# Kernel tuning notes

Hardware: AMD Instinct MI355X
Metric: run time of the kernel (lower is better)

## Reference

```python
import jax, jax.numpy as jnp
import numpy as np

TIME_SCALES = [1, 2, 4]
K = len(TIME_SCALES)      # 3 scales
N = 4                     # lcm(time_scales)
S = sum(TIME_SCALES)      # 7 slots
D_HEAD = 128              # d
D = S * D_HEAD            # 896
IO_DIM = 1024
RANK = 64
HIDDEN = 4 * D            # 3584
EPS = 1e-5


def _tables():
    active = np.empty((N, K), dtype=np.int64)
    perm = np.empty((N, K, N), dtype=np.int64)
    inv = np.empty((N, K, N), dtype=np.int64)
    ids = np.arange(N)
    for ph in range(N):
        off = 0
        for k, s in enumerate(TIME_SCALES):
            active[ph, k] = off + ph % s
            off += s
            j = ph % s
            alpha = N // s
            p = (ids + alpha * j) % N   # SHARED assignment
            perm[ph, k] = p
            ip = np.empty_like(p)
            ip[p] = ids
            inv[ph, k] = ip
    return active, perm, inv

ACTIVE, PERM, INV = _tables()


def _ln(x, scale, bias):
    mu = jnp.mean(x, axis=-1, keepdims=True)
    var = jnp.mean((x - mu) ** 2, axis=-1, keepdims=True)
    return (x - mu) * jax.lax.rsqrt(var + EPS) * scale + bias


def setup_inputs() -> dict:
    key = jax.random.key(0)
    ks = jax.random.split(key, 16)
    B, T = 8, 1024

    def w(k, shape, s=0.02):
        return jax.random.normal(k, shape, dtype=jnp.float32) * s

    return {
        "x": jax.random.normal(ks[0], (B, T, IO_DIM), dtype=jnp.float32),
        "enc_base_w": w(ks[1], (D, IO_DIM)),
        "enc_A_w": w(ks[2], (RANK, IO_DIM)),
        "enc_B": w(ks[3], (RANK, N, D)),
        "enc_beta": jnp.float32(0.01),
        "Wqkv": w(ks[4], (K, N, D_HEAD, 3 * D_HEAD)),
        "ln_attn_scale": jnp.ones((D_HEAD,), jnp.float32),
        "ln_attn_bias": jnp.zeros((D_HEAD,), jnp.float32),
        "ln_mixer_scale": jnp.ones((D,), jnp.float32),
        "ln_mixer_bias": jnp.zeros((D,), jnp.float32),
        "mixer_w1": w(ks[5], (HIDDEN, D)),
        "mixer_b1": jnp.zeros((HIDDEN,), jnp.float32),
        "mixer_w2": w(ks[6], (D, HIDDEN)),
        "mixer_b2": jnp.zeros((D,), jnp.float32),
        "dec_ln_scale": jnp.ones((N * D,), jnp.float32),
        "dec_ln_bias": jnp.zeros((N * D,), jnp.float32),
        "dec_down_w": w(ks[7], (RANK, N * D)),
        "dec_up_w": w(ks[8], (IO_DIM, RANK)),
        "phase": 1,
    }


def reference(x, enc_base_w, enc_A_w, enc_B, enc_beta, Wqkv,
              ln_attn_scale, ln_attn_bias, ln_mixer_scale, ln_mixer_bias,
              mixer_w1, mixer_b1, mixer_w2, mixer_b2,
              dec_ln_scale, dec_ln_bias, dec_down_w, dec_up_w, phase):
    B, T, _ = x.shape
    # ---- StreamLoRAEncoder: x [B,T,io] -> z0 [B,T,N,D]
    base = x @ enc_base_w.T                 # [B,T,D]
    h = x @ enc_A_w.T                       # [B,T,r]
    delta = jnp.einsum('btr,rnd->btnd', h, enc_B)
    z0 = base[:, :, None, :] + enc_beta * delta
    # ---- gather active slots for this phase (one slot per scale group)
    slots = ACTIVE[phase]                   # [K]
    z_slots = z0.reshape(B, T, N, S, D_HEAD)
    x_slot = z_slots[:, :, :, slots, :]     # [B,T,N,K,d]
    x_slot = _ln(x_slot, ln_attn_scale, ln_attn_bias)
    # ---- SHARED qkv projection (stream->head inverse perm, bmm, head->stream perm)
    x_in = x_slot.transpose(0, 1, 3, 2, 4)  # [B,T,K,N,d]
    kk = np.arange(K)[:, None]
    x_head = x_in[:, :, kk, INV[phase], :]  # [B,T,K,N,d]
    qkv = jnp.einsum('btknd,knde->btkne', x_head, Wqkv)  # [B,T,K,N,3d]
    qh, kh, vh = jnp.split(qkv, 3, axis=-1)
    p = PERM[phase]
    q = qh[:, :, kk, p, :].transpose(0, 3, 2, 1, 4).reshape(B, N * K, T, D_HEAD)
    k_ = kh[:, :, kk, p, :].transpose(0, 3, 2, 1, 4).reshape(B, N * K, T, D_HEAD)
    v = vh[:, :, kk, p, :].transpose(0, 3, 2, 1, 4).reshape(B, N * K, T, D_HEAD)
    # ---- causal attention over T per (stream, scale) head
    scores = jnp.einsum('bhtd,bhsd->bhts', q, k_) / np.float32(np.sqrt(D_HEAD))
    mask = jnp.tril(jnp.ones((T, T), dtype=bool))
    scores = jnp.where(mask, scores, jnp.float32(-1e9))
    attn = jax.nn.softmax(scores, axis=-1)
    out = jnp.einsum('bhts,bhsd->bhtd', attn, v)  # [B,N*K,T,d]
    # ---- scatter back to active slots (residual add)
    out5 = out.reshape(B, N, K, T, D_HEAD).transpose(0, 3, 1, 2, 4)  # [B,T,N,K,d]
    z1 = z_slots.at[:, :, :, slots, :].add(out5).reshape(B, T, N, D)
    # ---- mixer MLP (pre-LN residual)
    hm = _ln(z1, ln_mixer_scale, ln_mixer_bias)
    m = jax.nn.gelu(hm @ mixer_w1.T + mixer_b1, approximate=False) @ mixer_w2.T + mixer_b2
    z2 = z1 + m
    # ---- StreamLoRADecoder: concat streams, LN, rank-bottleneck projection
    cat = z2.reshape(B, T, N * D)
    y = _ln(cat, dec_ln_scale, dec_ln_bias) @ dec_down_w.T @ dec_up_w.T
    return y
```

## Files before the change

kernel.cpp:

```cpp
#include <hip/hip_runtime.h>
#include <hip/hip_bf16.h>
#include <math.h>


#define BT   8192
#define DH   128
#define DD   896
#define ND   3584
#define IO   1024
#define RK   64
#define HID  3584

typedef __attribute__((ext_vector_type(8))) short short8;
typedef __attribute__((ext_vector_type(4))) float f32x4;
typedef __hip_bfloat16 bf16;

#define DS_READ_B128(dst, p)                                                  \
    asm volatile("ds_read_b128 %0, %1"                                        \
                 : "=v"(dst)                                                  \
                 : "v"((const __attribute__((address_space(3))) bf16*)(p)))

__device__ __forceinline__ float gelu_f(float v)
{
    float u = v * 0.70710678118654752f;
    float a = fabsf(u);
    float t = __builtin_amdgcn_rcpf(1.0f + 0.3275911f * a);
    float p = t * (0.254829592f + t * (-0.284496736f + t * (1.421413741f +
              t * (-1.453152027f + t * 1.061405429f))));
    float er = 1.0f - p * __expf(-u * u);
    er = copysignf(er, u);
    return 0.5f * v * (1.0f + er);
}

template<int BM, int BN, int BK, int TM, int TN>
__global__ __launch_bounds__(256) void gemm_kernel(const float* __restrict__ A,
                                                   const float* __restrict__ B,
                                                   float* __restrict__ C,
                                                   int N, int Kd)
{
    constexpr int THREADS = (BM / TM) * (BN / TN);
    constexpr int LDA = BM + 4;
    constexpr int LDB = BN + 4;
    __shared__ float As[BK][LDA];
    __shared__ float Bs[BK][LDB];

    const int tid = threadIdx.x;
    constexpr int NX = BN / TN;
    const int tx = tid % NX;
    const int ty = tid / NX;
    const int row0 = blockIdx.y * BM;
    const int col0 = blockIdx.x * BN;

    float acc[TM][TN];
#pragma unroll
    for (int i = 0; i < TM; ++i)
#pragma unroll
        for (int j = 0; j < TN; ++j) acc[i][j] = 0.f;

    for (int k0 = 0; k0 < Kd; k0 += BK) {
        constexpr int AF4 = BM * BK / 4;
        for (int f = tid; f < AF4; f += THREADS) {
            int r  = f / (BK / 4);
            int c4 = (f % (BK / 4)) * 4;
            float4 v = *(const float4*)(A + (size_t)(row0 + r) * Kd + k0 + c4);
            As[c4 + 0][r] = v.x; As[c4 + 1][r] = v.y;
            As[c4 + 2][r] = v.z; As[c4 + 3][r] = v.w;
        }
        constexpr int BF4 = BN * BK / 4;
        for (int f = tid; f < BF4; f += THREADS) {
            int r  = f / (BK / 4);
            int c4 = (f % (BK / 4)) * 4;
            float4 v = *(const float4*)(B + (size_t)(col0 + r) * Kd + k0 + c4);
            Bs[c4 + 0][r] = v.x; Bs[c4 + 1][r] = v.y;
            Bs[c4 + 2][r] = v.z; Bs[c4 + 3][r] = v.w;
        }
        __syncthreads();

#pragma unroll
        for (int kk = 0; kk < BK; ++kk) {
            float a[TM], b[TN];
#pragma unroll
            for (int i = 0; i < TM; i += 4)
                *(float4*)&a[i] = *(const float4*)&As[kk][ty * TM + i];
#pragma unroll
            for (int j = 0; j < TN; j += 4)
                *(float4*)&b[j] = *(const float4*)&Bs[kk][tx * TN + j];
#pragma unroll
            for (int i = 0; i < TM; ++i)
#pragma unroll
                for (int j = 0; j < TN; ++j)
                    acc[i][j] = fmaf(a[i], b[j], acc[i][j]);
        }
        __syncthreads();
    }

    const int crow = row0 + ty * TM;
    const int ccol = col0 + tx * TN;
#pragma unroll
    for (int i = 0; i < TM; ++i) {
        float* cp = C + (size_t)(crow + i) * N + ccol;
#pragma unroll
        for (int j = 0; j < TN; ++j) cp[j] = acc[i][j];
    }
}

template<int SPLIT>
__global__ __launch_bounds__(256) void gemm_splitk_kernel(const float* __restrict__ A,
                                                          const float* __restrict__ B,
                                                          float* __restrict__ C,
                                                          int N, int ld)
{
    __shared__ float As[16][68];
    __shared__ float Bs[16][68];
    const int tid = threadIdx.x;
    const int tx = tid & 15, ty = tid >> 4;
    const int row0 = blockIdx.y * 64;
    const int col0 = blockIdx.x * 64;
    const int kn   = ld / SPLIT;
    const int kbeg = blockIdx.z * kn;

    float acc[4][4];
#pragma unroll
    for (int i = 0; i < 4; ++i)
#pragma unroll
        for (int j = 0; j < 4; ++j) acc[i][j] = 0.f;

    for (int k0 = kbeg; k0 < kbeg + kn; k0 += 16) {
        {
            int r = tid >> 2, c4 = (tid & 3) << 2;
            float4 v = *(const float4*)(A + (size_t)(row0 + r) * ld + k0 + c4);
            As[c4 + 0][r] = v.x; As[c4 + 1][r] = v.y;
            As[c4 + 2][r] = v.z; As[c4 + 3][r] = v.w;
            float4 w = *(const float4*)(B + (size_t)(col0 + r) * ld + k0 + c4);
            Bs[c4 + 0][r] = w.x; Bs[c4 + 1][r] = w.y;
            Bs[c4 + 2][r] = w.z; Bs[c4 + 3][r] = w.w;
        }
        __syncthreads();
#pragma unroll
        for (int kk = 0; kk < 16; ++kk) {
            float a[4], b[4];
            *(float4*)a = *(const float4*)&As[kk][ty * 4];
            *(float4*)b = *(const float4*)&Bs[kk][tx * 4];
#pragma unroll
            for (int i = 0; i < 4; ++i)
#pragma unroll
                for (int j = 0; j < 4; ++j)
                    acc[i][j] = fmaf(a[i], b[j], acc[i][j]);
        }
        __syncthreads();
    }

#pragma unroll
    for (int i = 0; i < 4; ++i)
#pragma unroll
        for (int j = 0; j < 4; ++j)
            atomicAdd(C + (size_t)(row0 + ty * 4 + i) * N + col0 + tx * 4 + j,
                      acc[i][j]);
}

template<int BN, int EPI>
__global__ __launch_bounds__(512, 2) void gemm_bf16_256(
    const bf16* __restrict__ A,
    const bf16* __restrict__ B,
    float* __restrict__ Cf,
    bf16* __restrict__ Cb,
    int N, int Kd,
    const float* __restrict__ bias)
{
    constexpr int NR    = BN / 64;
    constexpr int WTN   = 16 * NR;
    constexpr int ASLOT = 256 * 32;
    constexpr int BSLOT = BN * 32;
    __shared__ bf16 As[4 * ASLOT];
    __shared__ bf16 Bs[4 * BSLOT];

    const int tid  = threadIdx.x;
    const int wave = tid >> 6;
    const int lane = tid & 63;
    const int wm = wave >> 2, wn = wave & 3;
    const int lr = lane & 15, lq = lane >> 4;

    const int gx  = gridDim.x;
    int fid = blockIdx.y * gx + blockIdx.x;
    const int cpx = (gx * gridDim.y) >> 3;
    fid = (fid & 7) * cpx + (fid >> 3);
    const int row0 = (fid / gx) * 256;
    const int col0 = (fid % gx) * BN;

    const int sr  = lane >> 2;
    const int scs = (((lane & 3) ^ ((lane >> 3) & 3)) << 3);
    const bf16* Ag = A + (size_t)(row0 + sr) * Kd + scs;
    const bf16* Bg = B + (size_t)(col0 + sr) * Kd + scs;

    const int scox = (lq * 8) ^ (((lr >> 1) & 3) << 3);

    f32x4 acc[8][NR];
#pragma unroll
    for (int i = 0; i < 8; ++i)
#pragma unroll
        for (int j = 0; j < NR; ++j) acc[i][j] = (f32x4){0.f, 0.f, 0.f, 0.f};

    const int NH = Kd >> 5;

    auto stage = [&](int h) {
        const int slot = h & 3;
#pragma unroll
        for (int i = 0; i < 2; ++i) {
            const int rg = (i * 8 + wave) * 16;
            __builtin_amdgcn_global_load_lds(
                (const __attribute__((address_space(1))) unsigned int*)
                    (Ag + (size_t)rg * Kd + h * 32),
                (__attribute__((address_space(3))) unsigned int*)
                    (As + slot * ASLOT + rg * 32),
                16, 0, 0);
        }
#pragma unroll
        for (int i = 0; i < BN / 128; ++i) {
            const int rg = (i * 8 + wave) * 16;
            __builtin_amdgcn_global_load_lds(
                (const __attribute__((address_space(1))) unsigned int*)
                    (Bg + (size_t)rg * Kd + h * 32),
                (__attribute__((address_space(3))) unsigned int*)
                    (Bs + slot * BSLOT + rg * 32),
                16, 0, 0);
        }
    };

    stage(0); stage(1); stage(2);

    for (int h = 0; h < NH; ++h) {
        if (h + 3 < NH) stage(h + 3);

        const int ahead = NH - 1 - h;
        if constexpr (BN == 256) {
            if (ahead >= 3)      asm volatile("s_waitcnt vmcnt(12)" ::: "memory");
            else if (ahead == 2) asm volatile("s_waitcnt vmcnt(8)"  ::: "memory");
            else if (ahead == 1) asm volatile("s_waitcnt vmcnt(4)"  ::: "memory");
            else                 asm volatile("s_waitcnt vmcnt(0)"  ::: "memory");
        } else {
            if (ahead >= 3)      asm volatile("s_waitcnt vmcnt(9)"  ::: "memory");
            else if (ahead == 2) asm volatile("s_waitcnt vmcnt(6)"  ::: "memory");
            else if (ahead == 1) asm volatile("s_waitcnt vmcnt(3)"  ::: "memory");
            else                 asm volatile("s_waitcnt vmcnt(0)"  ::: "memory");
        }
        __builtin_amdgcn_s_barrier();

        const bf16* Ab = As + (h & 3) * ASLOT;
        const bf16* Bb = Bs + (h & 3) * BSLOT;

        short8 bfr[NR], afr[8];
#pragma unroll
        for (int nt = 0; nt < NR; ++nt)
            DS_READ_B128(bfr[nt], Bb + (wn * WTN + nt * 16 + lr) * 32 + scox);
#pragma unroll
        for (int mt = 0; mt < 8; ++mt)
            DS_READ_B128(afr[mt], Ab + (wm * 128 + mt * 16 + lr) * 32 + scox);

        asm volatile("s_waitcnt lgkmcnt(0)" ::: "memory");
        __builtin_amdgcn_sched_barrier(0);

        __builtin_amdgcn_s_setprio(1);
#pragma unroll
        for (int mt = 0; mt < 8; ++mt)
#pragma unroll
            for (int nt = 0; nt < NR; ++nt)
                acc[mt][nt] = __builtin_amdgcn_mfma_f32_16x16x32_bf16(
                    afr[mt], bfr[nt], acc[mt][nt], 0, 0, 0);
        __builtin_amdgcn_s_setprio(0);

        __builtin_amdgcn_s_barrier();
    }

#pragma unroll
    for (int mt = 0; mt < 8; ++mt) {
#pragma unroll
        for (int nt = 0; nt < NR; ++nt) {
            const int col = col0 + wn * WTN + nt * 16 + lr;
            const float bcol = (EPI == 0) ? 0.f : bias[col];
#pragma unroll
            for (int r = 0; r < 4; ++r) {
                const int row = row0 + wm * 128 + mt * 16 + lq * 4 + r;
                float v = acc[mt][nt][r] + bcol;
                if (EPI == 1) {
                    Cb[(size_t)row * N + col] = __float2bfloat16(gelu_f(v));
                } else if (EPI == 2) {
                    Cf[(size_t)row * N + col] += v;
                } else {
                    Cf[(size_t)row * N + col] = v;
                }
            }
        }
    }
}

__global__ __launch_bounds__(256) void pack_enc_kernel(const float* __restrict__ baseW,
                                                       const float* __restrict__ Aw,
                                                       const float* __restrict__ Bv,
                                                       const float* __restrict__ betap,
                                                       bf16* __restrict__ outp)
{
    __shared__ float Ps[64][68];
    __shared__ float Qs[64][68];
    const int tid = threadIdx.x;
    const int e0 = blockIdx.y * 64;
    const int k0 = blockIdx.x * 64;

    for (int f = tid; f < 1024; f += 256) {
        int r = f >> 4, c4 = (f & 15) << 2;
        *(float4*)&Ps[r][c4] = *(const float4*)(Bv + (size_t)r * ND + e0 + c4);
        *(float4*)&Qs[r][c4] = *(const float4*)(Aw + (size_t)r * IO + k0 + c4);
    }
    __syncthreads();

    const int tx = tid & 15, ty = tid >> 4;
    float acc[4][4];
#pragma unroll
    for (int i = 0; i < 4; ++i)
#pragma unroll
        for (int j = 0; j < 4; ++j) acc[i][j] = 0.f;

#pragma unroll 8
    for (int r = 0; r < 64; ++r) {
        float a[4], b[4];
        *(float4*)a = *(const float4*)&Ps[r][ty * 4];
        *(float4*)b = *(const float4*)&Qs[r][tx * 4];
#pragma unroll
        for (int i = 0; i < 4; ++i)
#pragma unroll
            for (int j = 0; j < 4; ++j) acc[i][j] = fmaf(a[i], b[j], acc[i][j]);
    }

    const float beta = betap[0];
#pragma unroll
    for (int i = 0; i < 4; ++i) {
        const int e = e0 + ty * 4 + i;
        const int d = e % DD;
#pragma unroll
        for (int j = 0; j < 4; ++j) {
            const int k = k0 + tx * 4 + j;
            float v = baseW[(size_t)d * IO + k] + beta * acc[i][j];
            outp[(size_t)e * IO + k] = __float2bfloat16(v);
        }
    }
}

__global__ __launch_bounds__(256) void qkv_bf16_kernel(
    const bf16* __restrict__ xh,
    const bf16* __restrict__ Wt,
    bf16* __restrict__ Qg,
    bf16* __restrict__ Kg,
    bf16* __restrict__ Vtg,
    const int* __restrict__ phase_p,
    int go)
{
    __shared__ bf16 As[128 * 64];
    __shared__ bf16 Bs[128 * 64];

    const int ph  = phase_p[0] & 3;
    const int zbl = blockIdx.z;
    const int hh  = (go + zbl) % 12;
    const int n   = hh / 3;
    const int k   = hh % 3;
    const int m   = (k == 0) ? n
                  : (k == 1) ? ((n + 2 * (ph & 1)) & 3)
                             : ((n + (ph & 3)) & 3);
    const bf16* A  = xh + (size_t)zbl * (1024 * 128);
    const bf16* Bw = Wt + (size_t)(k * 4 + m) * (384 * 128);

    const int tid  = threadIdx.x;
    const int wave = tid >> 6;
    const int lane = tid & 63;
    const int wm = wave >> 1, wn = wave & 1;
    const int row0 = blockIdx.y * 128;
    const int col0 = blockIdx.x * 128;
    const int lr = lane & 15;
    const int lq = lane >> 4;
    const int srow = lane >> 3;
    const int scol = (lane & 7) * 8;

    f32x4 acc[4][4];
#pragma unroll
    for (int i = 0; i < 4; ++i)
#pragma unroll
        for (int j = 0; j < 4; ++j) acc[i][j] = (f32x4){0.f, 0.f, 0.f, 0.f};

#pragma unroll
    for (int k0 = 0; k0 < 128; k0 += 64) {
#pragma unroll
        for (int j = 0; j < 4; ++j) {
            const int rg = wave * 32 + j * 8;
            __builtin_amdgcn_global_load_lds(
                (const __attribute__((address_space(1))) unsigned int*)
                    (A + (size_t)(row0 + rg + srow) * 128 + k0 + scol),
                (__attribute__((address_space(3))) unsigned int*)(As + rg * 64),
                16, 0, 0);
        }
#pragma unroll
        for (int j = 0; j < 4; ++j) {
            const int rg = wave * 32 + j * 8;
            __builtin_amdgcn_global_load_lds(
                (const __attribute__((address_space(1))) unsigned int*)
                    (Bw + (size_t)(col0 + rg + srow) * 128 + k0 + scol),
                (__attribute__((address_space(3))) unsigned int*)(Bs + rg * 64),
                16, 0, 0);
        }
        __syncthreads();

#pragma unroll
        for (int s = 0; s < 64; s += 32) {
            short8 af[4], bf[4];
#pragma unroll
            for (int mt = 0; mt < 4; ++mt)
                af[mt] = *(const short8*)&As[(wm * 64 + mt * 16 + lr) * 64 + s + lq * 8];
#pragma unroll
            for (int nt = 0; nt < 4; ++nt)
                bf[nt] = *(const short8*)&Bs[(wn * 64 + nt * 16 + lr) * 64 + s + lq * 8];
#pragma unroll
            for (int mt = 0; mt < 4; ++mt)
#pragma unroll
                for (int nt = 0; nt < 4; ++nt)
                    acc[mt][nt] = __builtin_amdgcn_mfma_f32_16x16x32_bf16(
                        af[mt], bf[nt], acc[mt][nt], 0, 0, 0);
        }
        __syncthreads();
    }

    if (col0 < 256) {
        bf16* C = (col0 == 0 ? Qg : Kg) + (size_t)zbl * (1024 * 128);
#pragma unroll
        for (int mt = 0; mt < 4; ++mt)
#pragma unroll
            for (int nt = 0; nt < 4; ++nt) {
                const int col = wn * 64 + nt * 16 + lr;
#pragma unroll
                for (int r = 0; r < 4; ++r) {
                    const int row = row0 + wm * 64 + mt * 16 + lq * 4 + r;
                    C[(size_t)row * 128 + col] = __float2bfloat16(acc[mt][nt][r]);
                }
            }
    } else {
        bf16* Vt = Vtg + (size_t)zbl * (128 * 1024);
#pragma unroll
        for (int mt = 0; mt < 4; ++mt)
#pragma unroll
            for (int nt = 0; nt < 4; ++nt) {
                const int d = wn * 64 + nt * 16 + lr;
                const int rowb = row0 + wm * 64 + mt * 16 + lq * 4;
                union { bf16 h[4]; uint2 u; } pk;
#pragma unroll
                for (int r = 0; r < 4; ++r)
                    pk.h[r] = __float2bfloat16(acc[mt][nt][r]);
                *(uint2*)(Vt + (size_t)d * 1024 + rowb) = pk.u;
            }
    }
}

__global__ __launch_bounds__(256) void flash_bf16_kernel(
    const bf16* __restrict__ Qg,
    const bf16* __restrict__ Kg,
    const bf16* __restrict__ Vtg,
    float* __restrict__ z,
    const int* __restrict__ phase_p,
    int go)
{
    __shared__ bf16 Ks[64 * 128];
    __shared__ bf16 Vs[128 * 64];
    __shared__ bf16 Ps[64 * 64];

    const int ph  = phase_p[0] & 3;
    const int zbl = blockIdx.x;
    const int zb  = go + zbl;
    const int b   = zb / 12;
    const int hh  = zb % 12;
    const int n   = hh / 3;
    const int ks  = hh % 3;
    const int slot = (ks == 0) ? 0 : (ks == 1 ? 1 + (ph & 1) : 3 + (ph & 3));
    const int q0  = blockIdx.y * 64;

    const bf16* Qp = Qg  + (size_t)zbl * (1024 * 128);
    const bf16* Kp = Kg  + (size_t)zbl * (1024 * 128);
    const bf16* Vp = Vtg + (size_t)zbl * (128 * 1024);

    const int tid  = threadIdx.x;
    const int wave = tid >> 6;
    const int lane = tid & 63;
    const int lr = lane & 15;
    const int lq = lane >> 4;
    const int sr4 = lane >> 4, sc4 = (lane & 15) * 8;
    const int sr8 = lane >> 3, sc8 = (lane & 7) * 8;
    const int swz = (lr & 7) << 3;

    short8 qreg[4];
#pragma unroll
    for (int s = 0; s < 4; ++s)
        qreg[s] = *(const short8*)(Qp + (size_t)(q0 + wave * 16 + lr) * 128
                                   + s * 32 + lq * 8);

    f32x4 accO[8];
    float m_i[4], l_i[4];
#pragma unroll
    for (int j = 0; j < 8; ++j) accO[j] = (f32x4){0.f, 0.f, 0.f, 0.f};
#pragma unroll
    for (int r = 0; r < 4; ++r) { m_i[r] = -1e30f; l_i[r] = 0.f; }
    const float sc = 0.08838834764831845f;

    for (int j0 = 0; j0 <= q0; j0 += 64) {
#pragma unroll
        for (int j = 0; j < 4; ++j) {
            const int rg = wave * 16 + j * 4;
            const int krow = rg + sr4;
            const int kcol = sc4 ^ ((krow & 7) << 3);
            __builtin_amdgcn_global_load_lds(
                (const __attribute__((address_space(1))) unsigned int*)
                    (Kp + (size_t)(j0 + krow) * 128 + kcol),
                (__attribute__((address_space(3))) unsigned int*)(Ks + rg * 128),
                16, 0, 0);
        }
#pragma unroll
        for (int j = 0; j < 4; ++j) {
            const int rg = wave * 32 + j * 8;
            const int vrow = rg + sr8;
            const int vcol = sc8 ^ ((vrow & 7) << 3);
            __builtin_amdgcn_global_load_lds(
                (const __attribute__((address_space(1))) unsigned int*)
                    (Vp + (size_t)vrow * 1024 + j0 + vcol),
                (__attribute__((address_space(3))) unsigned int*)(Vs + rg * 64),
                16, 0, 0);
        }
        __syncthreads();

        f32x4 accS[4];
#pragma unroll
        for (int nt = 0; nt < 4; ++nt) accS[nt] = (f32x4){0.f, 0.f, 0.f, 0.f};
#pragma unroll
        for (int s = 0; s < 4; ++s) {
            short8 bk[4];
#pragma unroll
            for (int nt = 0; nt < 4; ++nt)
                bk[nt] = *(const short8*)&Ks[(nt * 16 + lr) * 128
                                             + ((s * 32 + lq * 8) ^ swz)];
#pragma unroll
            for (int nt = 0; nt < 4; ++nt)
                accS[nt] = __builtin_amdgcn_mfma_f32_16x16x32_bf16(
                    qreg[s], bk[nt], accS[nt], 0, 0, 0);
        }

        const bool need_mask = (j0 == q0);
#pragma unroll
        for (int r = 0; r < 4; ++r) {
            const int row = q0 + wave * 16 + lq * 4 + r;
            float sv[4];
#pragma unroll
            for (int nt = 0; nt < 4; ++nt) {
                float v = accS[nt][r] * sc;
                if (need_mask && (j0 + nt * 16 + lr > row)) v = -1e30f;
                sv[nt] = v;
            }
            float mx = fmaxf(fmaxf(sv[0], sv[1]), fmaxf(sv[2], sv[3]));
#pragma unroll
            for (int msk = 8; msk; msk >>= 1) mx = fmaxf(mx, __shfl_xor(mx, msk, 16));
            float mnew = fmaxf(m_i[r], mx);
            float al   = __expf(m_i[r] - mnew);
            float rs = 0.f;
#pragma unroll
            for (int nt = 0; nt < 4; ++nt) {
                sv[nt] = __expf(sv[nt] - mnew);
                rs += sv[nt];
            }
#pragma unroll
            for (int msk = 8; msk; msk >>= 1) rs += __shfl_xor(rs, msk, 16);
            l_i[r] = l_i[r] * al + rs;
            m_i[r] = mnew;
#pragma unroll
            for (int d8 = 0; d8 < 8; ++d8) accO[d8][r] *= al;
            const int prow = wave * 16 + lq * 4 + r;
            const int pswz = (prow & 7) << 3;
#pragma unroll
            for (int nt = 0; nt < 4; ++nt)
                Ps[prow * 64 + ((nt * 16 + lr) ^ pswz)] = __float2bfloat16(sv[nt]);
        }

#pragma unroll
        for (int kvs = 0; kvs < 64; kvs += 32) {
            short8 ap = *(const short8*)&Ps[(wave * 16 + lr) * 64
                                            + ((kvs + lq * 8) ^ swz)];
            short8 bv[8];
#pragma unroll
            for (int d8 = 0; d8 < 8; ++d8)
                bv[d8] = *(const short8*)&Vs[(d8 * 16 + lr) * 64
                                             + ((kvs + lq * 8) ^ swz)];
#pragma unroll
            for (int d8 = 0; d8 < 8; ++d8)
                accO[d8] = __builtin_amdgcn_mfma_f32_16x16x32_bf16(
                    ap, bv[d8], accO[d8], 0, 0, 0);
        }
        __syncthreads();
    }

#pragma unroll
    for (int r = 0; r < 4; ++r) {
        const int t = q0 + wave * 16 + lq * 4 + r;
        const float inv = 1.0f / l_i[r];
        float* dst = z + (size_t)(b * 1024 + t) * ND + n * DD + slot * DH;
#pragma unroll
        for (int d8 = 0; d8 < 8; ++d8)
            dst[d8 * 16 + lr] += accO[d8][r] * inv;
    }
}

__global__ __launch_bounds__(256) void cvt_bf16_kernel(const float* __restrict__ src,
                                                       bf16* __restrict__ dst,
                                                       int n4)
{
    int i = blockIdx.x * 256 + threadIdx.x;
    if (i < n4) {
        float4 v = ((const float4*)src)[i];
        bf16* d = dst + (size_t)i * 4;
        d[0] = __float2bfloat16(v.x);
        d[1] = __float2bfloat16(v.y);
        d[2] = __float2bfloat16(v.z);
        d[3] = __float2bfloat16(v.w);
    }
}

__global__ __launch_bounds__(256) void cvt_wqkv_kernel(const float* __restrict__ W,
                                                       bf16* __restrict__ Wt)
{
    int o = blockIdx.x * 256 + threadIdx.x;
    if (o < 12 * 384 * 128) {
        int i = o / 49152, rem = o % 49152;
        int e = rem / 128, d = rem % 128;
        Wt[o] = __float2bfloat16(W[(size_t)i * 49152 + d * 384 + e]);
    }
}

__global__ __launch_bounds__(256) void ln_attn_kernel(const float* __restrict__ z,
                                                      bf16* __restrict__ xh,
                                                      const float* __restrict__ scale,
                                                      const float* __restrict__ bias,
                                                      const int* __restrict__ phase_p,
                                                      int bt0)
{
    const int ph   = phase_p[0] & 3;
    const int lane = threadIdx.x & 63;
    const int row  = blockIdx.x * 4 + (threadIdx.x >> 6);
    const int k    = row % 3;
    const int n    = (row / 3) & 3;
    const int btl  = row / 12;
    const int slot = (k == 0) ? 0 : (k == 1 ? 1 + (ph & 1) : 3 + (ph & 3));
    const int bt   = bt0 + btl;

    const float* src = z + (size_t)bt * ND + n * DD + slot * DH + lane * 2;
    float2 v = *(const float2*)src;
    float s = v.x + v.y;
    float q = v.x * v.x + v.y * v.y;
#pragma unroll
    for (int m = 32; m; m >>= 1) { s += __shfl_xor(s, m); q += __shfl_xor(q, m); }
    float mu  = s * (1.0f / 128.0f);
    float var = q * (1.0f / 128.0f) - mu * mu;
    float r   = rsqrtf(var + 1e-5f);

    float2 sc2 = *(const float2*)(scale + lane * 2);
    float2 bi2 = *(const float2*)(bias + lane * 2);
    const int bl = btl >> 10, t = btl & 1023;
    union { bf16 h[2]; unsigned int u; } pk;
    pk.h[0] = __float2bfloat16((v.x - mu) * r * sc2.x + bi2.x);
    pk.h[1] = __float2bfloat16((v.y - mu) * r * sc2.y + bi2.y);
    *(unsigned int*)(xh + (size_t)((bl * 12 + n * 3 + k) * 1024 + t) * DH + lane * 2) = pk.u;
}

template<int W>
__global__ __launch_bounds__(256) void ln_row_kernel(const float* __restrict__ in,
                                                     float* __restrict__ outp,
                                                     const float* __restrict__ scale,
                                                     const float* __restrict__ bias)
{
    constexpr int NIT = (W + 255) / 256;
    const int row = blockIdx.x;
    const int tid = threadIdx.x;
    const float* rp = in + (size_t)row * W;

    float v[NIT];
    float s = 0.f, q = 0.f;
#pragma unroll
    for (int i = 0; i < NIT; ++i) {
        int idx = tid + i * 256;
        if (idx < W) { float t = rp[idx]; v[i] = t; s += t; q += t * t; }
        else v[i] = 0.f;
    }
#pragma unroll
    for (int m = 32; m; m >>= 1) { s += __shfl_xor(s, m); q += __shfl_xor(q, m); }
    __shared__ float ss[4], sq[4];
    if ((tid & 63) == 0) { ss[tid >> 6] = s; sq[tid >> 6] = q; }
    __syncthreads();
    s = ss[0] + ss[1] + ss[2] + ss[3];
    q = sq[0] + sq[1] + sq[2] + sq[3];
    float mu  = s * (1.0f / W);
    float var = q * (1.0f / W) - mu * mu;
    float r   = rsqrtf(var + 1e-5f);

    float* op = outp + (size_t)row * W;
#pragma unroll
    for (int i = 0; i < NIT; ++i) {
        int idx = tid + i * 256;
        if (idx < W) op[idx] = (v[i] - mu) * r * scale[idx] + bias[idx];
    }
}

__global__ __launch_bounds__(256) void ln_row_bf16_kernel(const float* __restrict__ in,
                                                          bf16* __restrict__ outp,
                                                          const float* __restrict__ scale,
                                                          const float* __restrict__ bias)
{
    constexpr int W = 896, NIT = 4;
    const int row = blockIdx.x;
    const int tid = threadIdx.x;
    const float* rp = in + (size_t)row * W;

    float v[NIT];
    float s = 0.f, q = 0.f;
#pragma unroll
    for (int i = 0; i < NIT; ++i) {
        int idx = tid + i * 256;
        if (idx < W) { float t = rp[idx]; v[i] = t; s += t; q += t * t; }
        else v[i] = 0.f;
    }
#pragma unroll
    for (int m = 32; m; m >>= 1) { s += __shfl_xor(s, m); q += __shfl_xor(q, m); }
    __shared__ float ss[4], sq[4];
    if ((tid & 63) == 0) { ss[tid >> 6] = s; sq[tid >> 6] = q; }
    __syncthreads();
    s = ss[0] + ss[1] + ss[2] + ss[3];
    q = sq[0] + sq[1] + sq[2] + sq[3];
    float mu  = s * (1.0f / W);
    float var = q * (1.0f / W) - mu * mu;
    float r   = rsqrtf(var + 1e-5f);

    bf16* op = outp + (size_t)row * W;
#pragma unroll
    for (int i = 0; i < NIT; ++i) {
        int idx = tid + i * 256;
        if (idx < W)
            op[idx] = __float2bfloat16((v[i] - mu) * r * scale[idx] + bias[idx]);
    }
}

extern "C" void kernel_launch(void* const* d_in, const int* in_sizes, int n_in,
                              void* d_out, int out_size, void* d_ws, size_t ws_size,
                              hipStream_t stream)
{
    const float* x          = (const float*)d_in[0];
    const float* enc_base_w = (const float*)d_in[1];
    const float* enc_A_w    = (const float*)d_in[2];
    const float* enc_B      = (const float*)d_in[3];
    const float* enc_beta   = (const float*)d_in[4];
    const float* Wqkv       = (const float*)d_in[5];
    const float* ln_attn_s  = (const float*)d_in[6];
    const float* ln_attn_b  = (const float*)d_in[7];
    const float* ln_mix_s   = (const float*)d_in[8];
    const float* ln_mix_b   = (const float*)d_in[9];
    const float* w1         = (const float*)d_in[10];
    const float* b1         = (const float*)d_in[11];
    const float* w2         = (const float*)d_in[12];
    const float* b2         = (const float*)d_in[13];
    const float* dec_ln_s   = (const float*)d_in[14];
    const float* dec_ln_b   = (const float*)d_in[15];
    const float* dec_down   = (const float*)d_in[16];
    const float* dec_up     = (const float*)d_in[17];
    const int*   phase_p    = (const int*)d_in[18];
    float* out = (float*)d_out;

    float* ws = (float*)d_ws;
    float* z  = ws;
    float* R  = ws + (size_t)BT * ND;

    const int GQ = (ws_size >= 230000000UL) ? 96 : 48;
    const int CH = (ws_size >= 205000000UL) ? 8192 : 4096;

    bf16* xb   = (bf16*)R;
    bf16* Wenc = xb + (size_t)BT * IO;
    bf16* Wt   = (bf16*)R;
    bf16* xh_b = Wt + 12 * 384 * 128;
    bf16* Qb   = xh_b + (size_t)GQ * 1024 * 128;
    bf16* Kb   = Qb + (size_t)GQ * 1024 * 128;
    bf16* Vtg  = Kb + (size_t)GQ * 1024 * 128;
    bf16* w1b  = (bf16*)R;
    bf16* w2b  = w1b + (size_t)HID * DD;
    bf16* hm   = w2b + (size_t)DD * HID;
    bf16* gbuf = hm + (size_t)CH * DD;
    float* t1  = R;

    cvt_bf16_kernel<<<dim3(8192), 256, 0, stream>>>(x, xb, BT * IO / 4);
    pack_enc_kernel<<<dim3(16, 56), 256, 0, stream>>>(enc_base_w, enc_A_w, enc_B,
                                                      enc_beta, Wenc);
    gemm_bf16_256<256, 0><<<dim3(14, 32), 512, 0, stream>>>(xb, Wenc, z, nullptr,
                                                            ND, IO, nullptr);

    cvt_wqkv_kernel<<<dim3(2304), 256, 0, stream>>>(Wqkv, Wt);
    const int ngroups = 96 / GQ;
    for (int g = 0; g < ngroups; ++g) {
        ln_attn_kernel<<<dim3(GQ * 256), 256, 0, stream>>>(z, xh_b, ln_attn_s,
                                                           ln_attn_b, phase_p,
                                                           g * (GQ / 12) * 1024);
        qkv_bf16_kernel<<<dim3(3, 8, GQ), 256, 0, stream>>>(xh_b, Wt, Qb, Kb, Vtg,
                                                            phase_p, g * GQ);
        flash_bf16_kernel<<<dim3(GQ, 16), 256, 0, stream>>>(Qb, Kb, Vtg, z,
                                                            phase_p, g * GQ);
    }

    cvt_bf16_kernel<<<dim3(3136), 256, 0, stream>>>(w1, w1b, HID * DD / 4);
    cvt_bf16_kernel<<<dim3(3136), 256, 0, stream>>>(w2, w2b, DD * HID / 4);
    for (int c = 0; c < 32768 / CH; ++c) {
        float* zc = z + (size_t)c * CH * DD;
        ln_row_bf16_kernel<<<dim3(CH), 256, 0, stream>>>(zc, hm, ln_mix_s, ln_mix_b);
        gemm_bf16_256<256, 1><<<dim3(14, CH / 256), 512, 0, stream>>>(
            hm, w1b, nullptr, gbuf, HID, DD, b1);
        gemm_bf16_256<128, 2><<<dim3(7, CH / 256), 512, 0, stream>>>(
            gbuf, w2b, zc, nullptr, DD, HID, b2);
    }

    ln_row_kernel<3584><<<dim3(8192), 256, 0, stream>>>(z, z, dec_ln_s, dec_ln_b);
    hipMemsetAsync(t1, 0, (size_t)BT * RK * sizeof(float), stream);
    gemm_splitk_kernel<8><<<dim3(1, 128, 8), 256, 0, stream>>>(z, dec_down, t1,
                                                               RK, ND);
    gemm_kernel<128, 128, 16, 8, 8>
        <<<dim3(8, 64), 256, 0, stream>>>(t1, dec_up, out, IO, RK);
}
```

Baseline: 1.251 ms.

## Make flash attention persistent with atomic work queue and double-buffered KV loads

Turns the flash attention kernel into a persistent kernel of 512 blocks that pull (head, query-tile) items from an atomic counter, longest causal tiles first, to balance the triangular workload. K/V tiles are double-buffered in LDS so the next tile's global-to-LDS loads overlap the current tile's compute. LDS reads are software-pipelined with explicit waitcnts and sched barriers. LDS use doubles and a launch bound of 2 is set, which may limit occupancy, and the counters need a memset each run.

New measurement: 1.254 ms. About the same (+0.2%).

```diff
diff --git a/kernel.cpp b/kernel.cpp
--- a/kernel.cpp
+++ b/kernel.cpp
@@ -455,32 +455,20 @@
     }
 }
 
-__global__ __launch_bounds__(256) void flash_bf16_kernel(
+__global__ __launch_bounds__(256, 2) void flash_bf16_kernel(
     const bf16* __restrict__ Qg,
     const bf16* __restrict__ Kg,
     const bf16* __restrict__ Vtg,
     float* __restrict__ z,
     const int* __restrict__ phase_p,
-    int go)
-{
-    __shared__ bf16 Ks[64 * 128];
-    __shared__ bf16 Vs[128 * 64];
+    int go, int GQ, int* __restrict__ cnt)
+{
+    __shared__ bf16 Ks[2 * 64 * 128];
+    __shared__ bf16 Vs[2 * 128 * 64];
     __shared__ bf16 Ps[64 * 64];
-
-    const int ph  = phase_p[0] & 3;
-    const int zbl = blockIdx.x;
-    const int zb  = go + zbl;
-    const int b   = zb / 12;
-    const int hh  = zb % 12;
-    const int n   = hh / 3;
-    const int ks  = hh % 3;
-    const int slot = (ks == 0) ? 0 : (ks == 1 ? 1 + (ph & 1) : 3 + (ph & 3));
-    const int q0  = blockIdx.y * 64;
-
-    const bf16* Qp = Qg  + (size_t)zbl * (1024 * 128);
-    const bf16* Kp = Kg  + (size_t)zbl * (1024 * 128);
-    const bf16* Vp = Vtg + (size_t)zbl * (128 * 1024);
-
+    __shared__ int sw;
+
+    const int ph   = phase_p[0] & 3;
     const int tid  = threadIdx.x;
     const int wave = tid >> 6;
     const int lane = tid & 63;
@@ -489,122 +477,190 @@
     const int sr4 = lane >> 4, sc4 = (lane & 15) * 8;
     const int sr8 = lane >> 3, sc8 = (lane & 7) * 8;
     const int swz = (lr & 7) << 3;
-
-    short8 qreg[4];
-#pragma unroll
-    for (int s = 0; s < 4; ++s)
-        qreg[s] = *(const short8*)(Qp + (size_t)(q0 + wave * 16 + lr) * 128
-                                   + s * 32 + lq * 8);
-
-    f32x4 accO[8];
-    float m_i[4], l_i[4];
-#pragma unroll
-    for (int j = 0; j < 8; ++j) accO[j] = (f32x4){0.f, 0.f, 0.f, 0.f};
-#pragma unroll
-    for (int r = 0; r < 4; ++r) { m_i[r] = -1e30f; l_i[r] = 0.f; }
     const float sc = 0.08838834764831845f;
-
-    for (int j0 = 0; j0 <= q0; j0 += 64) {
-#pragma unroll
-        for (int j = 0; j < 4; ++j) {
-            const int rg = wave * 16 + j * 4;
-            const int krow = rg + sr4;
-            const int kcol = sc4 ^ ((krow & 7) << 3);
-            __builtin_amdgcn_global_load_lds(
-                (const __attribute__((address_space(1))) unsigned int*)
-                    (Kp + (size_t)(j0 + krow) * 128 + kcol),
-                (__attribute__((address_space(3))) unsigned int*)(Ks + rg * 128),
-                16, 0, 0);
-        }
-#pragma unroll
-        for (int j = 0; j < 4; ++j) {
-            const int rg = wave * 32 + j * 8;
-            const int vrow = rg + sr8;
-            const int vcol = sc8 ^ ((vrow & 7) << 3);
-            __builtin_amdgcn_global_load_lds(
-                (const __attribute__((address_space(1))) unsigned int*)
-                    (Vp + (size_t)vrow * 1024 + j0 + vcol),
-                (__attribute__((address_space(3))) unsigned int*)(Vs + rg * 64),
-                16, 0, 0);
-        }
+    const int nitems = GQ * 16;
+
+    for (;;) {
+        if (tid == 0) sw = atomicAdd(cnt, 1);
         __syncthreads();
-
-        f32x4 accS[4];
-#pragma unroll
-        for (int nt = 0; nt < 4; ++nt) accS[nt] = (f32x4){0.f, 0.f, 0.f, 0.f};
-#pragma unroll
-        for (int s = 0; s < 4; ++s) {
-            short8 bk[4];
+        const int w = sw;
+        if (w >= nitems) return;
+
+        const int wq  = w / GQ;
+        const int qy  = 15 - wq;
+        const int zbl = w - wq * GQ;
+        const int zb  = go + zbl;
+        const int b   = zb / 12;
+        const int hh  = zb % 12;
+        const int n   = hh / 3;
+        const int ksl = hh % 3;
+        const int slot = (ksl == 0) ? 0 : (ksl == 1 ? 1 + (ph & 1) : 3 + (ph & 3));
+        const int q0  = qy * 64;
+
+        const bf16* Qp = Qg  + (size_t)zbl * (1024 * 128);
+        const bf16* Kp = Kg  + (size_t)zbl * (1024 * 128);
+        const bf16* Vp = Vtg + (size_t)zbl * (128 * 1024);
+
+        auto stageKV = [&](int t) {
+            const int j0 = t * 64;
+            bf16* Kd = Ks + (t & 1) * (64 * 128);
+            bf16* Vd = Vs + (t & 1) * (128 * 64);
+#pragma unroll
+            for (int j = 0; j < 4; ++j) {
+                const int rg = wave * 16 + j * 4;
+                const int krow = rg + sr4;
+                const int kcol = sc4 ^ ((krow & 7) << 3);
+                __builtin_amdgcn_global_load_lds(
+                    (const __attribute__((address_space(1))) unsigned int*)
+                        (Kp + (size_t)(j0 + krow) * 128 + kcol),
+                    (__attribute__((address_space(3))) unsigned int*)(Kd + rg * 128),
+                    16, 0, 0);
+            }
+#pragma unroll
+            for (int j = 0; j < 4; ++j) {
+                const int rg = wave * 32 + j * 8;
+                const int vrow = rg + sr8;
+                const int vcol = sc8 ^ ((vrow & 7) << 3);
+                __builtin_amdgcn_global_load_lds(
+                    (const __attribute__((address_space(1))) unsigned int*)
+                        (Vp + (size_t)vrow * 1024 + j0 + vcol),
+                    (__attribute__((address_space(3))) unsigned int*)(Vd + rg * 64),
+                    16, 0, 0);
+            }
+        };
+
+        short8 qreg[4];
+#pragma unroll
+        for (int s = 0; s < 4; ++s)
+            qreg[s] = *(const short8*)(Qp + (size_t)(q0 + wave * 16 + lr) * 128
+                                       + s * 32 + lq * 8);
+
+        f32x4 accO[8];
+        float m_i[4], l_i[4];
+#pragma unroll
+        for (int j = 0; j < 8; ++j) accO[j] = (f32x4){0.f, 0.f, 0.f, 0.f};
+#pragma unroll
+        for (int r = 0; r < 4; ++r) { m_i[r] = -1e30f; l_i[r] = 0.f; }
+
+        const int NT = qy + 1;
+        stageKV(0);
+
+        for (int t = 0; t < NT; ++t) {
+            if (t + 1 < NT) {
+                stageKV(t + 1);
+                asm volatile("s_waitcnt vmcnt(8)" ::: "memory");
+            } else {
+                asm volatile("s_waitcnt vmcnt(0)" ::: "memory");
+            }
+            __builtin_amdgcn_s_barrier();
+            __builtin_amdgcn_sched_barrier(0);
+
+            const bf16* Kbb = Ks + (t & 1) * (64 * 128);
+            const bf16* Vbb = Vs + (t & 1) * (128 * 64);
+            const int j0 = t * 64;
+
+            f32x4 accS[4];
+#pragma unroll
+            for (int nt = 0; nt < 4; ++nt) accS[nt] = (f32x4){0.f, 0.f, 0.f, 0.f};
+            short8 bk[2][4];
 #pragma unroll
             for (int nt = 0; nt < 4; ++nt)
-                bk[nt] = *(const short8*)&Ks[(nt * 16 + lr) * 128
-                                             + ((s * 32 + lq * 8) ^ swz)];
-#pragma unroll
-            for (int nt = 0; nt < 4; ++nt)
-                accS[nt] = __builtin_amdgcn_mfma_f32_16x16x32_bf16(
-                    qreg[s], bk[nt], accS[nt], 0, 0, 0);
-        }
-
-        const bool need_mask = (j0 == q0);
+                DS_READ_B128(bk[0][nt],
+                             Kbb + (nt * 16 + lr) * 128 + ((lq * 8) ^ swz));
+#pragma unroll
+            for (int s = 0; s < 4; ++s) {
+                if (s + 1 < 4) {
+#pragma unroll
+                    for (int nt = 0; nt < 4; ++nt)
+                        DS_READ_B128(bk[(s + 1) & 1][nt],
+                                     Kbb + (nt * 16 + lr) * 128
+                                         + (((s + 1) * 32 + lq * 8) ^ swz));
+                    asm volatile("s_waitcnt lgkmcnt(4)" ::: "memory");
+                } else {
+                    asm volatile("s_waitcnt lgkmcnt(0)" ::: "memory");
+                }
+                __builtin_amdgcn_sched_barrier(0);
+#pragma unroll
+                for (int nt = 0; nt < 4; ++nt)
+                    accS[nt] = __builtin_amdgcn_mfma_f32_16x16x32_bf16(
+                        qreg[s], bk[s & 1][nt], accS[nt], 0, 0, 0);
+            }
+
+            const bool need_mask = (t == NT - 1);
+#pragma unroll
+            for (int r = 0; r < 4; ++r) {
+                const int row = q0 + wave * 16 + lq * 4 + r;
+                float sv[4];
+#pragma unroll
+                for (int nt = 0; nt < 4; ++nt) {
+                    float v = accS[nt][r] * sc;
+                    if (need_mask && (j0 + nt * 16 + lr > row)) v = -1e30f;
+                    sv[nt] = v;
+                }
+                float mx = fmaxf(fmaxf(sv[0], sv[1]), fmaxf(sv[2], sv[3]));
+#pragma unroll
+                for (int msk = 8; msk; msk >>= 1) mx = fmaxf(mx, __shfl_xor(mx, msk, 16));
+                float mnew = fmaxf(m_i[r], mx);
+                float al   = __expf(m_i[r] - mnew);
+                float rs = 0.f;
+#pragma unroll
+                for (int nt = 0; nt < 4; ++nt) {
+                    sv[nt] = __expf(sv[nt] - mnew);
+                    rs += sv[nt];
+                }
+#pragma unroll
+                for (int msk = 8; msk; msk >>= 1) rs += __shfl_xor(rs, msk, 16);
+                l_i[r] = l_i[r] * al + rs;
+                m_i[r] = mnew;
+#pragma unroll
+                for (int d8 = 0; d8 < 8; ++d8) accO[d8][r] *= al;
+                const int prow = wave * 16 + lq * 4 + r;
+                const int pswz = (prow & 7) << 3;
+#pragma unroll
+                for (int nt = 0; nt < 4; ++nt)
+                    Ps[prow * 64 + ((nt * 16 + lr) ^ pswz)] = __float2bfloat16(sv[nt]);
+            }
+            asm volatile("" ::: "memory");
+            __builtin_amdgcn_sched_barrier(0);
+
+            short8 ap[2], bv[2][8];
+            DS_READ_B128(ap[0], Ps + (wave * 16 + lr) * 64 + ((lq * 8) ^ swz));
+#pragma unroll
+            for (int d8 = 0; d8 < 8; ++d8)
+                DS_READ_B128(bv[0][d8],
+                             Vbb + (d8 * 16 + lr) * 64 + ((lq * 8) ^ swz));
+#pragma unroll
+            for (int kv = 0; kv < 2; ++kv) {
+                if (kv == 0) {
+                    DS_READ_B128(ap[1],
+                                 Ps + (wave * 16 + lr) * 64 + ((32 + lq * 8) ^ swz));
+#pragma unroll
+                    for (int d8 = 0; d8 < 8; ++d8)
+                        DS_READ_B128(bv[1][d8],
+                                     Vbb + (d8 * 16 + lr) * 64 + ((32 + lq * 8) ^ swz));
+                    asm volatile("s_waitcnt lgkmcnt(9)" ::: "memory");
+                } else {
+                    asm volatile("s_waitcnt lgkmcnt(0)" ::: "memory");
+                }
+                __builtin_amdgcn_sched_barrier(0);
+#pragma unroll
+                for (int d8 = 0; d8 < 8; ++d8)
+                    accO[d8] = __builtin_amdgcn_mfma_f32_16x16x32_bf16(
+                        ap[kv], bv[kv][d8], accO[d8], 0, 0, 0);
+            }
+
+            __builtin_amdgcn_s_barrier();
+        }
+
 #pragma unroll
         for (int r = 0; r < 4; ++r) {
-            const int row = q0 + wave * 16 + lq * 4 + r;
-            float sv[4];
-#pragma unroll
-            for (int nt = 0; nt < 4; ++nt) {
-                float v = accS[nt][r] * sc;
-                if (need_mask && (j0 + nt * 16 + lr > row)) v = -1e30f;
-                sv[nt] = v;
-            }
-            float mx = fmaxf(fmaxf(sv[0], sv[1]), fmaxf(sv[2], sv[3]));
-#pragma unroll
-            for (int msk = 8; msk; msk >>= 1) mx = fmaxf(mx, __shfl_xor(mx, msk, 16));
-            float mnew = fmaxf(m_i[r], mx);
-            float al   = __expf(m_i[r] - mnew);
-            float rs = 0.f;
-#pragma unroll
-            for (int nt = 0; nt < 4; ++nt) {
-                sv[nt] = __expf(sv[nt] - mnew);
-                rs += sv[nt];
-            }
-#pragma unroll
-            for (int msk = 8; msk; msk >>= 1) rs += __shfl_xor(rs, msk, 16);
-            l_i[r] = l_i[r] * al + rs;
-            m_i[r] = mnew;
-#pragma unroll
-            for (int d8 = 0; d8 < 8; ++d8) accO[d8][r] *= al;
-            const int prow = wave * 16 + lq * 4 + r;
-            const int pswz = (prow & 7) << 3;
-#pragma unroll
-            for (int nt = 0; nt < 4; ++nt)
-                Ps[prow * 64 + ((nt * 16 + lr) ^ pswz)] = __float2bfloat16(sv[nt]);
-        }
-
-#pragma unroll
-        for (int kvs = 0; kvs < 64; kvs += 32) {
-            short8 ap = *(const short8*)&Ps[(wave * 16 + lr) * 64
-                                            + ((kvs + lq * 8) ^ swz)];
-            short8 bv[8];
+            const int t = q0 + wave * 16 + lq * 4 + r;
+            const float inv = 1.0f / l_i[r];
+            float* dst = z + (size_t)(b * 1024 + t) * ND + n * DD + slot * DH;
 #pragma unroll
             for (int d8 = 0; d8 < 8; ++d8)
-                bv[d8] = *(const short8*)&Vs[(d8 * 16 + lr) * 64
-                                             + ((kvs + lq * 8) ^ swz)];
-#pragma unroll
-            for (int d8 = 0; d8 < 8; ++d8)
-                accO[d8] = __builtin_amdgcn_mfma_f32_16x16x32_bf16(
-                    ap, bv[d8], accO[d8], 0, 0, 0);
-        }
-        __syncthreads();
-    }
-
-#pragma unroll
-    for (int r = 0; r < 4; ++r) {
-        const int t = q0 + wave * 16 + lq * 4 + r;
-        const float inv = 1.0f / l_i[r];
-        float* dst = z + (size_t)(b * 1024 + t) * ND + n * DD + slot * DH;
-#pragma unroll
-        for (int d8 = 0; d8 < 8; ++d8)
-            dst[d8 * 16 + lr] += accO[d8][r] * inv;
+                dst[d8 * 16 + lr] += accO[d8][r] * inv;
+        }
     }
 }
 
@@ -784,6 +840,7 @@
     bf16* Qb   = xh_b + (size_t)GQ * 1024 * 128;
     bf16* Kb   = Qb + (size_t)GQ * 1024 * 128;
     bf16* Vtg  = Kb + (size_t)GQ * 1024 * 128;
+    int*  cnt  = (int*)(Vtg + (size_t)GQ * 128 * 1024);
     bf16* w1b  = (bf16*)R;
     bf16* w2b  = w1b + (size_t)HID * DD;
     bf16* hm   = w2b + (size_t)DD * HID;
@@ -797,6 +854,7 @@
                                                             ND, IO, nullptr);
 
     cvt_wqkv_kernel<<<dim3(2304), 256, 0, stream>>>(Wqkv, Wt);
+    hipMemsetAsync(cnt, 0, 2 * sizeof(int), stream);
     const int ngroups = 96 / GQ;
     for (int g = 0; g < ngroups; ++g) {
         ln_attn_kernel<<<dim3(GQ * 256), 256, 0, stream>>>(z, xh_b, ln_attn_s,
@@ -804,8 +862,9 @@
                                                            g * (GQ / 12) * 1024);
         qkv_bf16_kernel<<<dim3(3, 8, GQ), 256, 0, stream>>>(xh_b, Wt, Qb, Kb, Vtg,
                                                             phase_p, g * GQ);
-        flash_bf16_kernel<<<dim3(GQ, 16), 256, 0, stream>>>(Qb, Kb, Vtg, z,
-                                                            phase_p, g * GQ);
+        flash_bf16_kernel<<<dim3(512), 256, 0, stream>>>(Qb, Kb, Vtg, z,
+                                                         phase_p, g * GQ, GQ,
+                                                         cnt + g);
     }
 
     cvt_bf16_kernel<<<dim3(3136), 256, 0, stream>>>(w1, w1b, HID * DD / 4);
```
